# Kernel optimization log

Hardware: AMD Instinct MI355X
Metric: run time of the kernel (lower is better)

Reference implementation:

```python
import jax, jax.numpy as jnp
import numpy as np

D_MODEL = 1024
N_HEADS = 16
D_K = D_MODEL // N_HEADS
LN_EPS = 1e-5


def setup_inputs() -> dict:
    key = jax.random.key(0)
    ks = jax.random.split(key, 11)
    s = 1.0 / np.sqrt(D_MODEL)
    x = jax.random.normal(ks[0], (4, 2048, D_MODEL), dtype=jnp.float32)
    W_q = jax.random.uniform(ks[1], (D_MODEL, D_MODEL), jnp.float32, -s, s)
    b_q = jax.random.uniform(ks[2], (D_MODEL,), jnp.float32, -s, s)
    W_k = jax.random.uniform(ks[3], (D_MODEL, D_MODEL), jnp.float32, -s, s)
    b_k = jax.random.uniform(ks[4], (D_MODEL,), jnp.float32, -s, s)
    W_v = jax.random.uniform(ks[5], (D_MODEL, D_MODEL), jnp.float32, -s, s)
    b_v = jax.random.uniform(ks[6], (D_MODEL,), jnp.float32, -s, s)
    W_o = jax.random.uniform(ks[7], (D_MODEL, D_MODEL), jnp.float32, -s, s)
    b_o = jax.random.uniform(ks[8], (D_MODEL,), jnp.float32, -s, s)
    ln_gamma = jnp.ones((D_MODEL,), jnp.float32)
    ln_beta = jnp.zeros((D_MODEL,), jnp.float32)
    return {"x": x, "W_q": W_q, "b_q": b_q, "W_k": W_k, "b_k": b_k,
            "W_v": W_v, "b_v": b_v, "W_o": W_o, "b_o": b_o,
            "ln_gamma": ln_gamma, "ln_beta": ln_beta}


def reference(x, W_q, b_q, W_k, b_k, W_v, b_v, W_o, b_o, ln_gamma, ln_beta):
    B, S, D = x.shape
    # Linear projections (torch Linear: x @ W.T + b); split into heads.
    def proj(W, b):
        y = jnp.einsum('bsd,ed->bse', x, W) + b
        return y.reshape(B, S, N_HEADS, D_K).transpose(0, 2, 1, 3)  # [B,H,S,dk]
    Q = proj(W_q, b_q)
    K = proj(W_k, b_k)
    V = proj(W_v, b_v)
    scores = jnp.einsum('bhqd,bhkd->bhqk', Q, K) / np.sqrt(D_K)
    attn = jax.nn.softmax(scores, axis=-1)  # dropout is identity in eval
    context = jnp.einsum('bhqk,bhkd->bhqd', attn, V)
    context = context.transpose(0, 2, 1, 3).reshape(B, S, D)
    out = jnp.einsum('bsd,ed->bse', context, W_o) + b_o
    h = x + out  # residual
    mu = jnp.mean(h, axis=-1, keepdims=True)
    var = jnp.mean(jnp.square(h - mu), axis=-1, keepdims=True)
    return (h - mu) / jnp.sqrt(var + LN_EPS) * ln_gamma + ln_beta
```

## Files before the change

### kernel.cpp

```cpp
#include <hip/hip_runtime.h>
#include <hip/hip_bf16.h>
#include <stdint.h>

typedef __attribute__((ext_vector_type(4))) float f32x4;
typedef __attribute__((ext_vector_type(8))) short bf16x8;
typedef __attribute__((ext_vector_type(4))) short bf16x4;
typedef __attribute__((ext_vector_type(4))) short s16x4;

__device__ __forceinline__ float b2f(short s) {
    union { uint32_t u; float f; } v; v.u = ((uint32_t)(uint16_t)s) << 16; return v.f;
}
__device__ __forceinline__ short f2b(float f) {
    union { float f; uint32_t u; } v; v.f = f;
    uint32_t r = v.u + 0x7FFF + ((v.u >> 16) & 1);
    return (short)(r >> 16);
}
__device__ __forceinline__ f32x4 zero4() { f32x4 z = {0.f, 0.f, 0.f, 0.f}; return z; }

__device__ __forceinline__ void async16(const void* g, void* l) {
    __builtin_amdgcn_global_load_lds(
        (const __attribute__((address_space(1))) void*)g,
        (__attribute__((address_space(3))) void*)l, 16, 0, 0);
}
__device__ __forceinline__ uint32_t lds_addr(const void* p) {
    return (uint32_t)(uintptr_t)(const __attribute__((address_space(3))) void*)p;
}
__device__ __forceinline__ float exp2fast(float x) {
    float r; asm("v_exp_f32 %0, %1" : "=v"(r) : "v"(x)); return r;
}
__device__ __forceinline__ uint32_t cvtpk(float lo, float hi) {
    uint32_t r; asm("v_cvt_pk_bf16_f32 %0, %1, %2" : "=v"(r) : "v"(lo), "v"(hi)); return r;
}

__global__ __launch_bounds__(256)
void cvt5(const float* __restrict__ x,
          const float* __restrict__ wq, const float* __restrict__ wk,
          const float* __restrict__ wv, const float* __restrict__ wo,
          short* __restrict__ xb, short* __restrict__ wqb, short* __restrict__ wkb,
          short* __restrict__ wvb, short* __restrict__ wob)
{
    const int b = blockIdx.x;
    const float* src; short* dst; size_t off;
    if (b < 8192) { src = x; dst = xb; off = (size_t)b * 1024; }
    else {
        const int wsel = (b - 8192) >> 10;
        off = (size_t)((b - 8192) & 1023) * 1024;
        switch (wsel) {
            case 0: src = wq; dst = wqb; break;
            case 1: src = wk; dst = wkb; break;
            case 2: src = wv; dst = wvb; break;
            default: src = wo; dst = wob; break;
        }
    }
    const int t = threadIdx.x;
    const float4 v = *(const float4*)(src + off + t * 4);
    s16x4 o;
    o[0] = f2b(v.x); o[1] = f2b(v.y); o[2] = f2b(v.z); o[3] = f2b(v.w);
    *(s16x4*)(dst + off + t * 4) = o;
}

template <bool OUTF32, bool RESID>
__device__ __forceinline__
void gemm_core(const short* __restrict__ Ab, const short* __restrict__ Bb,
               const float* __restrict__ bias, const float* __restrict__ resid,
               void* __restrict__ Cv, int m0, int n0col, int K, int N,
               short* lsA, short* lsB)
{
    const int t = threadIdx.x;
    const int wave = t >> 6, lane = t & 63;
    const int wr = wave >> 1, wc = wave & 1;
    const int lr = lane & 15, kg = lane >> 4;

    f32x4 acc[4][4];
#pragma unroll
    for (int m = 0; m < 4; ++m)
#pragma unroll
        for (int n = 0; n < 4; ++n) acc[m][n] = zero4();

    const int r0 = t >> 2;
    const int c0 = (t & 3) * 8;

    async16(Ab + (size_t)r0 * K + c0,        &lsA[t * 8]);
    async16(Ab + (size_t)(r0 + 64) * K + c0, &lsA[t * 8 + 2048]);
    async16(Bb + (size_t)r0 * K + c0,        &lsB[t * 8]);
    async16(Bb + (size_t)(r0 + 64) * K + c0, &lsB[t * 8 + 2048]);
    __syncthreads();

    int buf = 0;
    for (int k0 = 0; k0 < K; k0 += 32) {
        if (k0 + 32 < K) {
            const int kn = k0 + 32;
            short* dA = lsA + (buf ^ 1) * 4096;
            short* dB = lsB + (buf ^ 1) * 4096;
            async16(Ab + (size_t)r0 * K + kn + c0,        dA + t * 8);
            async16(Ab + (size_t)(r0 + 64) * K + kn + c0, dA + t * 8 + 2048);
            async16(Bb + (size_t)r0 * K + kn + c0,        dB + t * 8);
            async16(Bb + (size_t)(r0 + 64) * K + kn + c0, dB + t * 8 + 2048);
        }

        const short* cA = lsA + buf * 4096;
        const short* cB = lsB + buf * 4096;
        bf16x8 aF[4], bF[4];
#pragma unroll
        for (int m = 0; m < 4; ++m)
            aF[m] = *(const bf16x8*)&cA[(wr * 64 + m * 16 + lr) * 32 + kg * 8];
#pragma unroll
        for (int n = 0; n < 4; ++n)
            bF[n] = *(const bf16x8*)&cB[(wc * 64 + n * 16 + lr) * 32 + kg * 8];
#pragma unroll
        for (int m = 0; m < 4; ++m)
#pragma unroll
            for (int n = 0; n < 4; ++n)
                acc[m][n] = __builtin_amdgcn_mfma_f32_16x16x32_bf16(aF[m], bF[n], acc[m][n], 0, 0, 0);

        __syncthreads();
        buf ^= 1;
    }

#pragma unroll
    for (int n = 0; n < 4; ++n) {
        const int col = n0col + wc * 64 + n * 16 + lr;
        const float bvv = bias[col];
#pragma unroll
        for (int m = 0; m < 4; ++m) {
            const int rowb = m0 + wr * 64 + m * 16 + kg * 4;
#pragma unroll
            for (int r = 0; r < 4; ++r) {
                const size_t idx = (size_t)(rowb + r) * N + col;
                float v = acc[m][n][r] + bvv;
                if (RESID) v += resid[idx];
                if (OUTF32) ((float*)Cv)[idx] = v;
                else        ((short*)Cv)[idx] = f2b(v);
            }
        }
    }
}

__global__ __launch_bounds__(256)
void gemm_qkv(const short* __restrict__ A, const short* __restrict__ Wcat,
              const float* __restrict__ bq, const float* __restrict__ bk,
              const float* __restrict__ bv,
              short* __restrict__ Qw, short* __restrict__ Kw, short* __restrict__ Vw)
{
    __shared__ short lsA[2 * 128 * 32];
    __shared__ short lsB[2 * 128 * 32];
    const int L = blockIdx.x;
    const int wgid = (L & 7) * 192 + (L >> 3);
    const int nb = wgid % 24;
    const int my = wgid / 24;
    const int tb = nb >> 3;
    const float* bias = (tb == 0) ? bq : (tb == 1) ? bk : bv;
    short* dst = (tb == 0) ? Qw : (tb == 1) ? Kw : Vw;
    gemm_core<false, false>(A + (size_t)my * 128 * 1024,
                            Wcat + (size_t)nb * 128 * 1024,
                            bias - (nb & 7) * 128,
                            nullptr, dst, my * 128, (nb & 7) * 128, 1024, 1024,
                            lsA, lsB);
}

__global__ __launch_bounds__(256)
void gemm_out(const short* __restrict__ A, const short* __restrict__ Bw,
              const float* __restrict__ bias, const float* __restrict__ resid,
              float* __restrict__ C)
{
    __shared__ short lsA[2 * 128 * 32];
    __shared__ short lsB[2 * 128 * 32];
    const int L = blockIdx.x;
    const int wgid = (L & 7) * 64 + (L >> 3);
    const int nb = wgid & 7, my = wgid >> 3;
    gemm_core<true, true>(A + (size_t)my * 128 * 1024,
                          Bw + (size_t)nb * 128 * 1024,
                          bias, resid, C, my * 128, nb * 128, 1024, 1024,
                          lsA, lsB);
}

__global__ __launch_bounds__(512)
void attn_fwd(const short* __restrict__ Q, const short* __restrict__ K,
              const short* __restrict__ V, short* __restrict__ ctx)
{
    __shared__ short lsK[2][64 * 64];
    __shared__ short lsV[2][64 * 64];
    __shared__ short lsP[8][16 * 64];

    const float C1 = 0.18033688011112042f;

    const int t = threadIdx.x, w = t >> 6, lane = t & 63;
    const int lr = lane & 15, kg = lane >> 4;
    const int bh = blockIdx.x;
    const size_t base = (size_t)(bh >> 4) * 2048 * 1024 + (size_t)(bh & 15) * 64;
    const short* Qg = Q + base;
    short* Og = ctx + base;
    const int q0 = blockIdx.y * 256 + w * 32;

    bf16x8 qB[2][2];
#pragma unroll
    for (int m = 0; m < 2; ++m)
#pragma unroll
        for (int ks = 0; ks < 2; ++ks)
            qB[m][ks] = *(const bf16x8*)(Qg + (size_t)(q0 + m * 16 + lr) * 1024 + ks * 32 + kg * 8);

    bf16x8 onesB;
#pragma unroll
    for (int j = 0; j < 8; ++j) onesB[j] = (short)0x3F80;

    const int rK  = t >> 3;
    const int cK  = (((t & 7) ^ (rK & 7))) * 8;
    const int kvV = (t & 127) >> 1;
    const int dV  = ((t >> 7) << 4) + (t & 1) * 8;
    const short* pK = K + base + (size_t)rK * 1024 + cK;
    const short* pV = V + base + (size_t)kvV * 1024 + dV;

    f32x4 o[2][4];
    f32x4 osum[2];
#pragma unroll
    for (int m = 0; m < 2; ++m) {
#pragma unroll
        for (int n = 0; n < 4; ++n) o[m][n] = zero4();
        osum[m] = zero4();
    }
    float mx[2] = {-1e30f, -1e30f};

    const int pmask = (lr & 7) << 3;
    short* lsPw = lsP[w];

    async16(pK, &lsK[0][t * 8]);
    async16(pV, &lsV[0][t * 8]);

    int buf = 0;
    for (int it = 0; it < 32; ++it) {
        __syncthreads();
        if (it + 1 < 32) {
            pK += 65536; pV += 65536;
            async16(pK, &lsK[buf ^ 1][t * 8]);
            async16(pV, &lsV[buf ^ 1][t * 8]);
        }
        const short* cbK = lsK[buf];
        const short* cbV = lsV[buf];

        f32x4 s[2][4];
        const int x0 = ((kg)     ^ (lr & 7)) * 8;
        const int x1 = ((4 + kg) ^ (lr & 7)) * 8;
        __builtin_amdgcn_s_setprio(1);
#pragma unroll
        for (int cb = 0; cb < 4; ++cb) {
            const bf16x8 kA0 = *(const bf16x8*)&cbK[(cb * 16 + lr) * 64 + x0];
            const bf16x8 kA1 = *(const bf16x8*)&cbK[(cb * 16 + lr) * 64 + x1];
#pragma unroll
            for (int m = 0; m < 2; ++m) {
                f32x4 a = __builtin_amdgcn_mfma_f32_16x16x32_bf16(kA0, qB[m][0], zero4(), 0, 0, 0);
                s[m][cb] = __builtin_amdgcn_mfma_f32_16x16x32_bf16(kA1, qB[m][1], a, 0, 0, 0);
            }
        }
        __builtin_amdgcn_s_setprio(0);

        float smax[2];
#pragma unroll
        for (int m = 0; m < 2; ++m) {
            float a = fmaxf(fmaxf(s[m][0][0], s[m][0][1]), fmaxf(s[m][0][2], s[m][0][3]));
            float b = fmaxf(fmaxf(s[m][1][0], s[m][1][1]), fmaxf(s[m][1][2], s[m][1][3]));
            float c = fmaxf(fmaxf(s[m][2][0], s[m][2][1]), fmaxf(s[m][2][2], s[m][2][3]));
            float d = fmaxf(fmaxf(s[m][3][0], s[m][3][1]), fmaxf(s[m][3][2], s[m][3][3]));
            float e = fmaxf(fmaxf(a, b), fmaxf(c, d));
            e = fmaxf(e, __shfl_xor(e, 16));
            e = fmaxf(e, __shfl_xor(e, 32));
            smax[m] = e;
        }

        if (!__all((smax[0] <= mx[0] + 64.f) && (smax[1] <= mx[1] + 64.f))) {
            float corrS[2];
#pragma unroll
            for (int m = 0; m < 2; ++m) {
                const float mnew = fmaxf(mx[m], smax[m]);
                corrS[m] = exp2fast((mx[m] - mnew) * C1);
                mx[m] = mnew;
            }
#pragma unroll
            for (int m = 0; m < 2; ++m) {
                f32x4 c;
#pragma unroll
                for (int r = 0; r < 4; ++r) c[r] = __shfl(corrS[m], kg * 4 + r);
#pragma unroll
                for (int n = 0; n < 4; ++n) {
                    o[m][n][0] *= c[0]; o[m][n][1] *= c[1];
                    o[m][n][2] *= c[2]; o[m][n][3] *= c[3];
                }
                osum[m][0] *= c[0]; osum[m][1] *= c[1];
                osum[m][2] *= c[2]; osum[m][3] *= c[3];
            }
        }

        bf16x4 tv[4][4];
#pragma unroll
        for (int n = 0; n < 4; ++n) {
            const uint32_t a = lds_addr(&cbV[n * 1024 + kg * 128 + lr]);
            asm volatile(
                "ds_read_b64_tr_b16 %0, %4\n\t"
                "ds_read_b64_tr_b16 %1, %4 offset:128\n\t"
                "ds_read_b64_tr_b16 %2, %4 offset:1024\n\t"
                "ds_read_b64_tr_b16 %3, %4 offset:1152"
                : "=&v"(tv[n][0]), "=&v"(tv[n][1]), "=&v"(tv[n][2]), "=&v"(tv[n][3])
                : "v"(a));
        }
        asm volatile("s_waitcnt lgkmcnt(0)" ::: "memory");
        __builtin_amdgcn_sched_barrier(0);

#pragma unroll
        for (int m = 0; m < 2; ++m) {
            const float nm2 = mx[m] * C1;
#pragma unroll
            for (int cb = 0; cb < 4; ++cb) {
                const float p0 = exp2fast(fmaf(s[m][cb][0], C1, -nm2));
                const float p1 = exp2fast(fmaf(s[m][cb][1], C1, -nm2));
                const float p2 = exp2fast(fmaf(s[m][cb][2], C1, -nm2));
                const float p3 = exp2fast(fmaf(s[m][cb][3], C1, -nm2));
                const int c0i = (cb * 16 + kg * 4) ^ pmask;
                *(uint32_t*)&lsPw[lr * 64 + c0i]     = cvtpk(p0, p1);
                *(uint32_t*)&lsPw[lr * 64 + c0i + 2] = cvtpk(p2, p3);
            }

            bf16x8 pA[2];
#pragma unroll
            for (int kh = 0; kh < 2; ++kh)
                pA[kh] = *(const bf16x8*)&lsPw[lr * 64 + ((kh * 32 + kg * 8) ^ pmask)];

            __builtin_amdgcn_s_setprio(1);
#pragma unroll
            for (int n = 0; n < 4; ++n) {
#pragma unroll
                for (int kh = 0; kh < 2; ++kh) {
                    const bf16x8 vB = __builtin_shufflevector(tv[n][kh * 2], tv[n][kh * 2 + 1],
                                                              0, 1, 2, 3, 4, 5, 6, 7);
                    o[m][n] = __builtin_amdgcn_mfma_f32_16x16x32_bf16(pA[kh], vB, o[m][n], 0, 0, 0);
                }
            }
            osum[m] = __builtin_amdgcn_mfma_f32_16x16x32_bf16(pA[0], onesB, osum[m], 0, 0, 0);
            osum[m] = __builtin_amdgcn_mfma_f32_16x16x32_bf16(pA[1], onesB, osum[m], 0, 0, 0);
            __builtin_amdgcn_s_setprio(0);
        }
        buf ^= 1;
    }

#pragma unroll
    for (int m = 0; m < 2; ++m) {
        f32x4 inv;
#pragma unroll
        for (int r = 0; r < 4; ++r) inv[r] = 1.0f / osum[m][r];
#pragma unroll
        for (int n = 0; n < 4; ++n)
#pragma unroll
            for (int r = 0; r < 4; ++r) {
                const int row = q0 + m * 16 + kg * 4 + r;
                Og[(size_t)row * 1024 + n * 16 + lr] = f2b(o[m][n][r] * inv[r]);
            }
    }
}

__global__ __launch_bounds__(256)
void ln_inplace(float* __restrict__ io, const float* __restrict__ gamma,
                const float* __restrict__ beta)
{
    __shared__ float redS[4];
    __shared__ float redQ[4];
    const int t = threadIdx.x, wave = t >> 6, lane = t & 63;
    const size_t rb = (size_t)blockIdx.x * 1024;

    float4 v4 = *(const float4*)&io[rb + t * 4];
    float v[4] = {v4.x, v4.y, v4.z, v4.w};

    float s = 0.f, sq = 0.f;
#pragma unroll
    for (int j = 0; j < 4; ++j) { s += v[j]; sq += v[j] * v[j]; }
#pragma unroll
    for (int off = 32; off; off >>= 1) {
        s  += __shfl_xor(s, off);
        sq += __shfl_xor(sq, off);
    }
    if (lane == 0) { redS[wave] = s; redQ[wave] = sq; }
    __syncthreads();
    const float mean = (redS[0] + redS[1] + redS[2] + redS[3]) * (1.0f / 1024.0f);
    const float ex2  = (redQ[0] + redQ[1] + redQ[2] + redQ[3]) * (1.0f / 1024.0f);
    const float var  = fmaxf(ex2 - mean * mean, 0.f);
    const float inv  = rsqrtf(var + 1e-5f);

    float4 o4;
    o4.x = (v[0] - mean) * inv * gamma[t * 4 + 0] + beta[t * 4 + 0];
    o4.y = (v[1] - mean) * inv * gamma[t * 4 + 1] + beta[t * 4 + 1];
    o4.z = (v[2] - mean) * inv * gamma[t * 4 + 2] + beta[t * 4 + 2];
    o4.w = (v[3] - mean) * inv * gamma[t * 4 + 3] + beta[t * 4 + 3];
    *(float4*)&io[rb + t * 4] = o4;
}

extern "C" void kernel_launch(void* const* d_in, const int* in_sizes, int n_in,
                              void* d_out, int out_size, void* d_ws, size_t ws_size,
                              hipStream_t stream)
{
    const float* x  = (const float*)d_in[0];
    const float* Wq = (const float*)d_in[1];
    const float* bq = (const float*)d_in[2];
    const float* Wk = (const float*)d_in[3];
    const float* bk = (const float*)d_in[4];
    const float* Wv = (const float*)d_in[5];
    const float* bv = (const float*)d_in[6];
    const float* Wo = (const float*)d_in[7];
    const float* bo = (const float*)d_in[8];
    const float* gamma = (const float*)d_in[9];
    const float* beta  = (const float*)d_in[10];

    const size_t NX = (size_t)8192 * 1024;
    const size_t NW = (size_t)1024 * 1024;

    short* xb  = (short*)d_ws;
    short* Wqb = xb + NX;
    short* Wkb = Wqb + NW;
    short* Wvb = Wkb + NW;
    short* Wob = Wvb + NW;
    short* Qw  = Wob + NW;
    short* Kw  = Qw + NX;
    short* Vw  = Kw + NX;
    short* Cw  = Vw + NX;
    float* out = (float*)d_out;

    cvt5<<<dim3(12288), dim3(256), 0, stream>>>(x, Wq, Wk, Wv, Wo, xb, Wqb, Wkb, Wvb, Wob);
    gemm_qkv<<<dim3(1536), dim3(256), 0, stream>>>(xb, Wqb, bq, bk, bv, Qw, Kw, Vw);
    attn_fwd<<<dim3(64, 8), dim3(512), 0, stream>>>(Qw, Kw, Vw, Cw);
    gemm_out<<<dim3(512), dim3(256), 0, stream>>>(Cw, Wob, bo, x, out);
    ln_inplace<<<dim3(8192), dim3(256), 0, stream>>>(out, gamma, beta);
}
```

Baseline: 242.0 us.

## Split attention KV range in two and merge partials in a combine kernel

The attention kernel now launches a second grid dimension of two, so each block covers half of the key/value sequence (16 tiles instead of 32). Each block writes its normalized partial context plus per-row max and sum. A new combine kernel rescales and merges the two partials, reusing the freed x and Wq bf16 buffers as scratch. This doubles the block count (512 to 1024) to fill more compute units, at the cost of an extra pass over the context, the side-buffer traffic, and bf16 rounding of the partials.

```diff
diff --git a/kernel.cpp b/kernel.cpp
--- a/kernel.cpp
+++ b/kernel.cpp
@@ -176,7 +176,8 @@
 
 __global__ __launch_bounds__(512)
 void attn_fwd(const short* __restrict__ Q, const short* __restrict__ K,
-              const short* __restrict__ V, short* __restrict__ ctx)
+              const short* __restrict__ V, short* __restrict__ part0,
+              short* __restrict__ part1, float2* __restrict__ side)
 {
     __shared__ short lsK[2][64 * 64];
     __shared__ short lsV[2][64 * 64];
@@ -187,9 +188,10 @@
     const int t = threadIdx.x, w = t >> 6, lane = t & 63;
     const int lr = lane & 15, kg = lane >> 4;
     const int bh = blockIdx.x;
+    const int z  = blockIdx.z;
     const size_t base = (size_t)(bh >> 4) * 2048 * 1024 + (size_t)(bh & 15) * 64;
     const short* Qg = Q + base;
-    short* Og = ctx + base;
+    short* Og = (z ? part1 : part0) + base;
     const int q0 = blockIdx.y * 256 + w * 32;
 
     bf16x8 qB[2][2];
@@ -207,8 +209,9 @@
     const int cK  = (((t & 7) ^ (rK & 7))) * 8;
     const int kvV = (t & 127) >> 1;
     const int dV  = ((t >> 7) << 4) + (t & 1) * 8;
-    const short* pK = K + base + (size_t)rK * 1024 + cK;
-    const short* pV = V + base + (size_t)kvV * 1024 + dV;
+    const size_t zoff = (size_t)z << 20;
+    const short* pK = K + base + zoff + (size_t)rK * 1024 + cK;
+    const short* pV = V + base + zoff + (size_t)kvV * 1024 + dV;
 
     f32x4 o[2][4];
     f32x4 osum[2];
@@ -227,9 +230,9 @@
     async16(pV, &lsV[0][t * 8]);
 
     int buf = 0;
-    for (int it = 0; it < 32; ++it) {
+    for (int it = 0; it < 16; ++it) {
         __syncthreads();
-        if (it + 1 < 32) {
+        if (it + 1 < 16) {
             pK += 65536; pV += 65536;
             async16(pK, &lsK[buf ^ 1][t * 8]);
             async16(pV, &lsV[buf ^ 1][t * 8]);
@@ -340,11 +343,24 @@
         buf ^= 1;
     }
 
+    const int head = bh & 15;
+    const size_t rowg = (size_t)(bh >> 4) * 2048;
 #pragma unroll
     for (int m = 0; m < 2; ++m) {
-        f32x4 inv;
-#pragma unroll
-        for (int r = 0; r < 4; ++r) inv[r] = 1.0f / osum[m][r];
+        f32x4 inv, mxr;
+#pragma unroll
+        for (int r = 0; r < 4; ++r) {
+            inv[r] = 1.0f / osum[m][r];
+            mxr[r] = __shfl(mx[m], kg * 4 + r);
+        }
+        if (lr == 0) {
+#pragma unroll
+            for (int r = 0; r < 4; ++r) {
+                const size_t row = rowg + q0 + m * 16 + kg * 4 + r;
+                side[((size_t)z * 8192 + row) * 16 + head] =
+                    make_float2(mxr[r], osum[m][r]);
+            }
+        }
 #pragma unroll
         for (int n = 0; n < 4; ++n)
 #pragma unroll
@@ -353,6 +369,31 @@
                 Og[(size_t)row * 1024 + n * 16 + lr] = f2b(o[m][n][r] * inv[r]);
             }
     }
+}
+
+__global__ __launch_bounds__(256)
+void attn_combine(short* __restrict__ part0, const short* __restrict__ part1,
+                  const float2* __restrict__ side)
+{
+    const float C1 = 0.18033688011112042f;
+    const int row = blockIdx.x;
+    const int t = threadIdx.x;
+    const int head = t >> 4;
+    const float2 s1 = side[(size_t)row * 16 + head];
+    const float2 s2 = side[(size_t)(8192 + row) * 16 + head];
+    const float M = fmaxf(s1.x, s2.x);
+    const float w1 = exp2fast((s1.x - M) * C1) * s1.y;
+    const float w2 = exp2fast((s2.x - M) * C1) * s2.y;
+    const float inv = 1.0f / (w1 + w2);
+    const float a1 = w1 * inv, a2 = w2 * inv;
+    const size_t idx = (size_t)row * 1024 + t * 4;
+    s16x4 p1 = *(const s16x4*)&part0[idx];
+    s16x4 p2 = *(const s16x4*)&part1[idx];
+    s16x4 o;
+#pragma unroll
+    for (int j = 0; j < 4; ++j)
+        o[j] = f2b(b2f(p1[j]) * a1 + b2f(p2[j]) * a2);
+    *(s16x4*)&part0[idx] = o;
 }
 
 __global__ __launch_bounds__(256)
@@ -420,9 +461,13 @@
     short* Cw  = Vw + NX;
     float* out = (float*)d_out;
 
+    short*  part1 = xb;
+    float2* side  = (float2*)Wqb;
+
     cvt5<<<dim3(12288), dim3(256), 0, stream>>>(x, Wq, Wk, Wv, Wo, xb, Wqb, Wkb, Wvb, Wob);
     gemm_qkv<<<dim3(1536), dim3(256), 0, stream>>>(xb, Wqb, bq, bk, bv, Qw, Kw, Vw);
-    attn_fwd<<<dim3(64, 8), dim3(512), 0, stream>>>(Qw, Kw, Vw, Cw);
+    attn_fwd<<<dim3(64, 8, 2), dim3(512), 0, stream>>>(Qw, Kw, Vw, Cw, part1, side);
+    attn_combine<<<dim3(8192), dim3(256), 0, stream>>>(Cw, part1, side);
     gemm_out<<<dim3(512), dim3(256), 0, stream>>>(Cw, Wob, bo, x, out);
     ln_inplace<<<dim3(8192), dim3(256), 0, stream>>>(out, gamma, beta);
 }
```

Result: slower. 260.1 us (+7.5%).
